# Optimization experiments

Measured on AMD Instinct MI355X. Metric: run time of the kernel, lower is better.

The kernel has to match this reference:

```python
import jax, jax.numpy as jnp
import numpy as np

N_NODES = 200000
D = 128            # in_channels
B_GRAPHS = 512     # batch_size
STEPS = 3          # processing_steps


def setup_inputs() -> dict:
    key = jax.random.key(0)
    k = jax.random.split(key, 6)
    x = jax.random.normal(k[0], (N_NODES, D), dtype=jnp.float32)
    batch = jnp.sort(jax.random.randint(k[1], (N_NODES,), 0, B_GRAPHS, dtype=jnp.int64))
    s = 0.1
    W_ih = jax.random.normal(k[2], (3 * D, 2 * D), dtype=jnp.float32) * s
    W_hh = jax.random.normal(k[3], (3 * D, D), dtype=jnp.float32) * s
    b_ih = jax.random.normal(k[4], (3 * D,), dtype=jnp.float32) * s
    b_hh = jax.random.normal(k[5], (3 * D,), dtype=jnp.float32) * s
    return {"x": x, "batch": batch, "batch_size": B_GRAPHS,
            "W_ih": W_ih, "W_hh": W_hh, "b_ih": b_ih, "b_hh": b_hh}


def _gru_cell(inp, h, W_ih, W_hh, b_ih, b_hh):
    # inp: [B, 2d], h: [B, d]; PyTorch GRU gate order: r, z, n
    gi = inp @ W_ih.T + b_ih  # [B, 3d]
    gh = h @ W_hh.T + b_hh    # [B, 3d]
    gi_r, gi_z, gi_n = jnp.split(gi, 3, axis=-1)
    gh_r, gh_z, gh_n = jnp.split(gh, 3, axis=-1)
    r = jax.nn.sigmoid(gi_r + gh_r)
    z = jax.nn.sigmoid(gi_z + gh_z)
    n = jnp.tanh(gi_n + r * gh_n)
    return (1.0 - z) * n + z * h


def reference(x, batch, batch_size, W_ih, W_hh, b_ih, b_hh):
    B = batch_size
    d = x.shape[1]
    h = jnp.zeros((B, d), dtype=x.dtype)
    q_star = jnp.zeros((B, 2 * d), dtype=x.dtype)
    for _ in range(STEPS):
        h = _gru_cell(q_star, h, W_ih, W_hh, b_ih, b_hh)
        q = h  # num_layers=1: output == new hidden state
        e = jnp.sum(x * q[batch], axis=-1)  # [N]
        m = jax.ops.segment_max(e, batch, num_segments=B)
        ex = jnp.exp(e - m[batch])
        s = jax.ops.segment_sum(ex, batch, num_segments=B)
        a = ex / (s[batch] + 1e-16)  # segment softmax weights [N]
        r = jax.ops.segment_sum(a[:, None] * x, batch, num_segments=B)  # [B, d]
        q_star = jnp.concatenate([q, r], axis=-1)
    return q_star
```

## Files before the change

kernel.cpp:

```cpp
#include <hip/hip_runtime.h>
#include <math.h>

constexpr int D = 128;
constexpr int B = 512;
constexpr int STEPS = 3;
constexpr int NW_IH = 3 * D * 2 * D;
constexpr int NW_HH = 3 * D * D;

__device__ __forceinline__ float sigmoidf_(float x) { return 1.f / (1.f + __expf(-x)); }
__device__ __forceinline__ float bflo(unsigned int u) { return __uint_as_float(u << 16); }
__device__ __forceinline__ float bfhi(unsigned int u) { return __uint_as_float(u & 0xffff0000u); }
__device__ __forceinline__ unsigned short f2bf_rn(float f) {
    unsigned int u = __float_as_uint(f);
    u += 0x7fffu + ((u >> 16) & 1u);
    return (unsigned short)(u >> 16);
}

__global__ __launch_bounds__(256) void k_prep(const float* __restrict__ Wih,
        const float* __restrict__ Whh, const int* __restrict__ batch, int n,
        unsigned short* __restrict__ wih_bf, unsigned short* __restrict__ whh_bf,
        int* __restrict__ seg) {
    int i = blockIdx.x * blockDim.x + threadIdx.x;
    if (i < NW_IH) wih_bf[i] = f2bf_rn(Wih[i]);
    else if (i < NW_IH + NW_HH) whh_bf[i - NW_IH] = f2bf_rn(Whh[i - NW_IH]);
    if (i <= B) {
        int lo = 0, hi = n;
        while (lo < hi) { int mid = (lo + hi) >> 1; if (batch[mid] < i) lo = mid + 1; else hi = mid; }
        seg[i] = lo;
    }
}

__global__ __launch_bounds__(1024, 8) void k_set2set(
        const float* __restrict__ x,
        const unsigned short* __restrict__ wih_bf,
        const unsigned short* __restrict__ whh_bf,
        const float* __restrict__ bih, const float* __restrict__ bhh,
        const int* __restrict__ seg, float* __restrict__ out) {
    __shared__ float s_q[2 * D];
    __shared__ float s_h[D];
    __shared__ float s_gi[3 * D], s_gh[3 * D];
    __shared__ float sm[32], sl[32];
    __shared__ float s_M, s_inv;
    __shared__ float rpart[16][D];

    const int b = blockIdx.x;
    const int tid = threadIdx.x;
    const int start = seg[b], end = seg[b + 1];
    const int lane32 = tid & 31;
    const int hw = tid >> 5;

    if (tid < 2 * D) s_q[tid] = 0.f;
    if (tid < D) s_h[tid] = 0.f;
    __syncthreads();

    for (int step = 0; step < STEPS; ++step) {
        if (tid < 3 * D) {
            const int t = tid;
            float gi = bih[t], gh = bhh[t];
            const uint4* wr = (const uint4*)(wih_bf + (size_t)t * (2 * D));
#pragma unroll 2
            for (int c = 0; c < (2 * D) / 8; ++c) {
                uint4 w = wr[c];
                const float* q = &s_q[c * 8];
                gi = fmaf(bflo(w.x), q[0], gi); gi = fmaf(bfhi(w.x), q[1], gi);
                gi = fmaf(bflo(w.y), q[2], gi); gi = fmaf(bfhi(w.y), q[3], gi);
                gi = fmaf(bflo(w.z), q[4], gi); gi = fmaf(bfhi(w.z), q[5], gi);
                gi = fmaf(bflo(w.w), q[6], gi); gi = fmaf(bfhi(w.w), q[7], gi);
            }
            const uint4* vr = (const uint4*)(whh_bf + (size_t)t * D);
#pragma unroll 2
            for (int c = 0; c < D / 8; ++c) {
                uint4 w = vr[c];
                const float* hh = &s_h[c * 8];
                gh = fmaf(bflo(w.x), hh[0], gh); gh = fmaf(bfhi(w.x), hh[1], gh);
                gh = fmaf(bflo(w.y), hh[2], gh); gh = fmaf(bfhi(w.y), hh[3], gh);
                gh = fmaf(bflo(w.z), hh[4], gh); gh = fmaf(bfhi(w.z), hh[5], gh);
                gh = fmaf(bflo(w.w), hh[6], gh); gh = fmaf(bfhi(w.w), hh[7], gh);
            }
            s_gi[t] = gi; s_gh[t] = gh;
        }
        __syncthreads();
        if (tid < D) {
            const int t = tid;
            float r  = sigmoidf_(s_gi[t] + s_gh[t]);
            float z  = sigmoidf_(s_gi[D + t] + s_gh[D + t]);
            float nn = tanhf(s_gi[2 * D + t] + r * s_gh[2 * D + t]);
            float hn = (1.f - z) * nn + z * s_h[t];
            s_h[t] = hn;
            s_q[t] = hn;
        }
        __syncthreads();

        const float4 qf = *(const float4*)&s_h[lane32 * 4];
        float m_run = -INFINITY, l_run = 0.f;
        float4 acc = {0.f, 0.f, 0.f, 0.f};
        for (int node = start + hw; node < end; node += 32) {
            float4 xv = ((const float4*)(x + (size_t)node * D))[lane32];
            float p = fmaf(xv.x, qf.x, fmaf(xv.y, qf.y, fmaf(xv.z, qf.z, xv.w * qf.w)));
            p += __shfl_xor(p, 16, 64);
            p += __shfl_xor(p, 8, 64);
            p += __shfl_xor(p, 4, 64);
            p += __shfl_xor(p, 2, 64);
            p += __shfl_xor(p, 1, 64);
            float nm = fmaxf(m_run, p);
            float scale = __expf(m_run - nm);
            float a = __expf(p - nm);
            l_run = fmaf(l_run, scale, a);
            acc.x = fmaf(acc.x, scale, a * xv.x);
            acc.y = fmaf(acc.y, scale, a * xv.y);
            acc.z = fmaf(acc.z, scale, a * xv.z);
            acc.w = fmaf(acc.w, scale, a * xv.w);
            m_run = nm;
        }
        if (lane32 == 0) { sm[hw] = m_run; sl[hw] = l_run; }
        __syncthreads();
        if (tid == 0) {
            float M = -INFINITY;
            for (int i = 0; i < 32; ++i) M = fmaxf(M, sm[i]);
            float L = 0.f;
            for (int i = 0; i < 32; ++i)
                L += (sm[i] == -INFINITY) ? 0.f : sl[i] * __expf(sm[i] - M);
            s_M = M;
            s_inv = 1.f / (L + 1e-16f);
        }
        __syncthreads();
        const float fac = (m_run == -INFINITY) ? 0.f : __expf(m_run - s_M);
        acc.x *= fac; acc.y *= fac; acc.z *= fac; acc.w *= fac;
        acc.x += __shfl_down(acc.x, 32, 64);
        acc.y += __shfl_down(acc.y, 32, 64);
        acc.z += __shfl_down(acc.z, 32, 64);
        acc.w += __shfl_down(acc.w, 32, 64);
        const int wave = tid >> 6;
        const int lane64 = tid & 63;
        if (lane64 < 32) ((float4*)rpart[wave])[lane64] = acc;
        __syncthreads();
        if (tid < D) {
            float v = 0.f;
#pragma unroll
            for (int w = 0; w < 16; ++w) v += rpart[w][tid];
            s_q[D + tid] = v * s_inv;
        }
        __syncthreads();
    }

    if (tid < 2 * D) out[(size_t)b * (2 * D) + tid] = s_q[tid];
}

extern "C" void kernel_launch(void* const* d_in, const int* in_sizes, int n_in,
                              void* d_out, int out_size, void* d_ws, size_t ws_size,
                              hipStream_t stream) {
    const float* x    = (const float*)d_in[0];
    const int*   batch= (const int*)d_in[1];
    const float* Wih  = (const float*)d_in[3];
    const float* Whh  = (const float*)d_in[4];
    const float* bih  = (const float*)d_in[5];
    const float* bhh  = (const float*)d_in[6];
    const int n = in_sizes[0] / D;

    char* ws = (char*)d_ws;
    int* seg = (int*)ws;
    unsigned short* wih_bf = (unsigned short*)(ws + 4096);
    unsigned short* whh_bf = (unsigned short*)(ws + 4096 + (size_t)NW_IH * 2);

    const int total = NW_IH + NW_HH;
    k_prep<<<(total + 255) / 256, 256, 0, stream>>>(Wih, Whh, batch, n, wih_bf, whh_bf, seg);
    k_set2set<<<B, 1024, 0, stream>>>(x, wih_bf, whh_bf, bih, bhh, seg, (float*)d_out);
}
```

Before: 250.8 us.

## Split fused Set2Set kernel into per-step GRU and split-segment attention kernels

Replaces the single persistent kernel (one 1024-thread block per graph running all steps) with a loop of launches per step: a GRU kernel, an attention kernel that splits each graph's nodes into four chunks across 2048 blocks of 256 threads and writes partial softmax stats, and a final combine kernel. The aim is higher occupancy and better load balance for the memory-bound node scan over x. The GRU dot products now use four independent accumulators to shorten the FMA dependency chain. The cost is seven extra launches and partial results round-tripping through global memory between steps.

```diff
diff --git a/kernel.cpp b/kernel.cpp
--- a/kernel.cpp
+++ b/kernel.cpp
@@ -30,120 +30,175 @@
     }
 }
 
-__global__ __launch_bounds__(1024, 8) void k_set2set(
-        const float* __restrict__ x,
+__global__ __launch_bounds__(384) void k_cg(
         const unsigned short* __restrict__ wih_bf,
         const unsigned short* __restrict__ whh_bf,
         const float* __restrict__ bih, const float* __restrict__ bhh,
-        const int* __restrict__ seg, float* __restrict__ out) {
+        float* __restrict__ g_h,
+        const float* __restrict__ Pm, const float* __restrict__ Pl,
+        const float* __restrict__ Pacc, int first) {
     __shared__ float s_q[2 * D];
     __shared__ float s_h[D];
     __shared__ float s_gi[3 * D], s_gh[3 * D];
-    __shared__ float sm[32], sl[32];
-    __shared__ float s_M, s_inv;
-    __shared__ float rpart[16][D];
-
-    const int b = blockIdx.x;
+    const int g = blockIdx.x;
+    const int t = threadIdx.x;
+
+    if (t < D) {
+        float hp = first ? 0.f : g_h[(size_t)g * D + t];
+        s_h[t] = hp;
+        s_q[t] = hp;
+        float r = 0.f;
+        if (!first) {
+            float m0 = Pm[g * 4 + 0], m1 = Pm[g * 4 + 1];
+            float m2 = Pm[g * 4 + 2], m3 = Pm[g * 4 + 3];
+            float M = fmaxf(fmaxf(m0, m1), fmaxf(m2, m3));
+            float w0 = (m0 == -INFINITY) ? 0.f : __expf(m0 - M);
+            float w1 = (m1 == -INFINITY) ? 0.f : __expf(m1 - M);
+            float w2 = (m2 == -INFINITY) ? 0.f : __expf(m2 - M);
+            float w3 = (m3 == -INFINITY) ? 0.f : __expf(m3 - M);
+            float l = w0 * Pl[g * 4 + 0] + w1 * Pl[g * 4 + 1]
+                    + w2 * Pl[g * 4 + 2] + w3 * Pl[g * 4 + 3];
+            float inv = 1.f / (l + 1e-16f);
+            r = (w0 * Pacc[(size_t)(g * 4 + 0) * D + t]
+               + w1 * Pacc[(size_t)(g * 4 + 1) * D + t]
+               + w2 * Pacc[(size_t)(g * 4 + 2) * D + t]
+               + w3 * Pacc[(size_t)(g * 4 + 3) * D + t]) * inv;
+        }
+        s_q[D + t] = r;
+    }
+    __syncthreads();
+
+    {
+        float a0 = bih[t], a1 = 0.f, a2 = 0.f, a3 = 0.f;
+        const uint4* wr = (const uint4*)(wih_bf + (size_t)t * (2 * D));
+#pragma unroll 4
+        for (int c = 0; c < (2 * D) / 8; ++c) {
+            uint4 w = wr[c];
+            const float* q = &s_q[c * 8];
+            a0 = fmaf(bflo(w.x), q[0], a0); a0 = fmaf(bfhi(w.x), q[1], a0);
+            a1 = fmaf(bflo(w.y), q[2], a1); a1 = fmaf(bfhi(w.y), q[3], a1);
+            a2 = fmaf(bflo(w.z), q[4], a2); a2 = fmaf(bfhi(w.z), q[5], a2);
+            a3 = fmaf(bflo(w.w), q[6], a3); a3 = fmaf(bfhi(w.w), q[7], a3);
+        }
+        s_gi[t] = (a0 + a1) + (a2 + a3);
+        float b0 = bhh[t], b1 = 0.f, b2 = 0.f, b3 = 0.f;
+        const uint4* vr = (const uint4*)(whh_bf + (size_t)t * D);
+#pragma unroll 4
+        for (int c = 0; c < D / 8; ++c) {
+            uint4 w = vr[c];
+            const float* hh = &s_h[c * 8];
+            b0 = fmaf(bflo(w.x), hh[0], b0); b0 = fmaf(bfhi(w.x), hh[1], b0);
+            b1 = fmaf(bflo(w.y), hh[2], b1); b1 = fmaf(bfhi(w.y), hh[3], b1);
+            b2 = fmaf(bflo(w.z), hh[4], b2); b2 = fmaf(bfhi(w.z), hh[5], b2);
+            b3 = fmaf(bflo(w.w), hh[6], b3); b3 = fmaf(bfhi(w.w), hh[7], b3);
+        }
+        s_gh[t] = (b0 + b1) + (b2 + b3);
+    }
+    __syncthreads();
+
+    if (t < D) {
+        float r  = sigmoidf_(s_gi[t] + s_gh[t]);
+        float z  = sigmoidf_(s_gi[D + t] + s_gh[D + t]);
+        float nn = tanhf(s_gi[2 * D + t] + r * s_gh[2 * D + t]);
+        float hn = (1.f - z) * nn + z * s_h[t];
+        g_h[(size_t)g * D + t] = hn;
+    }
+}
+
+__global__ __launch_bounds__(256, 8) void k_attn_p(const float* __restrict__ x,
+        const float* __restrict__ g_h, const int* __restrict__ seg,
+        float* __restrict__ Pm, float* __restrict__ Pl,
+        float* __restrict__ Pacc) {
+    const int bid = blockIdx.x;
+    const int g = bid >> 2, j = bid & 3;
+    const int s = seg[g], e = seg[g + 1];
+    const int len = e - s;
+    const int qs = s + (len * j) / 4;
+    const int qe = s + (len * (j + 1)) / 4;
+
     const int tid = threadIdx.x;
-    const int start = seg[b], end = seg[b + 1];
     const int lane32 = tid & 31;
     const int hw = tid >> 5;
 
-    if (tid < 2 * D) s_q[tid] = 0.f;
-    if (tid < D) s_h[tid] = 0.f;
-    __syncthreads();
-
-    for (int step = 0; step < STEPS; ++step) {
-        if (tid < 3 * D) {
-            const int t = tid;
-            float gi = bih[t], gh = bhh[t];
-            const uint4* wr = (const uint4*)(wih_bf + (size_t)t * (2 * D));
-#pragma unroll 2
-            for (int c = 0; c < (2 * D) / 8; ++c) {
-                uint4 w = wr[c];
-                const float* q = &s_q[c * 8];
-                gi = fmaf(bflo(w.x), q[0], gi); gi = fmaf(bfhi(w.x), q[1], gi);
-                gi = fmaf(bflo(w.y), q[2], gi); gi = fmaf(bfhi(w.y), q[3], gi);
-                gi = fmaf(bflo(w.z), q[4], gi); gi = fmaf(bfhi(w.z), q[5], gi);
-                gi = fmaf(bflo(w.w), q[6], gi); gi = fmaf(bfhi(w.w), q[7], gi);
-            }
-            const uint4* vr = (const uint4*)(whh_bf + (size_t)t * D);
-#pragma unroll 2
-            for (int c = 0; c < D / 8; ++c) {
-                uint4 w = vr[c];
-                const float* hh = &s_h[c * 8];
-                gh = fmaf(bflo(w.x), hh[0], gh); gh = fmaf(bfhi(w.x), hh[1], gh);
-                gh = fmaf(bflo(w.y), hh[2], gh); gh = fmaf(bfhi(w.y), hh[3], gh);
-                gh = fmaf(bflo(w.z), hh[4], gh); gh = fmaf(bfhi(w.z), hh[5], gh);
-                gh = fmaf(bflo(w.w), hh[6], gh); gh = fmaf(bfhi(w.w), hh[7], gh);
-            }
-            s_gi[t] = gi; s_gh[t] = gh;
-        }
-        __syncthreads();
-        if (tid < D) {
-            const int t = tid;
-            float r  = sigmoidf_(s_gi[t] + s_gh[t]);
-            float z  = sigmoidf_(s_gi[D + t] + s_gh[D + t]);
-            float nn = tanhf(s_gi[2 * D + t] + r * s_gh[2 * D + t]);
-            float hn = (1.f - z) * nn + z * s_h[t];
-            s_h[t] = hn;
-            s_q[t] = hn;
-        }
-        __syncthreads();
-
-        const float4 qf = *(const float4*)&s_h[lane32 * 4];
-        float m_run = -INFINITY, l_run = 0.f;
-        float4 acc = {0.f, 0.f, 0.f, 0.f};
-        for (int node = start + hw; node < end; node += 32) {
-            float4 xv = ((const float4*)(x + (size_t)node * D))[lane32];
-            float p = fmaf(xv.x, qf.x, fmaf(xv.y, qf.y, fmaf(xv.z, qf.z, xv.w * qf.w)));
-            p += __shfl_xor(p, 16, 64);
-            p += __shfl_xor(p, 8, 64);
-            p += __shfl_xor(p, 4, 64);
-            p += __shfl_xor(p, 2, 64);
-            p += __shfl_xor(p, 1, 64);
-            float nm = fmaxf(m_run, p);
-            float scale = __expf(m_run - nm);
-            float a = __expf(p - nm);
-            l_run = fmaf(l_run, scale, a);
-            acc.x = fmaf(acc.x, scale, a * xv.x);
-            acc.y = fmaf(acc.y, scale, a * xv.y);
-            acc.z = fmaf(acc.z, scale, a * xv.z);
-            acc.w = fmaf(acc.w, scale, a * xv.w);
-            m_run = nm;
-        }
-        if (lane32 == 0) { sm[hw] = m_run; sl[hw] = l_run; }
-        __syncthreads();
-        if (tid == 0) {
-            float M = -INFINITY;
-            for (int i = 0; i < 32; ++i) M = fmaxf(M, sm[i]);
-            float L = 0.f;
-            for (int i = 0; i < 32; ++i)
-                L += (sm[i] == -INFINITY) ? 0.f : sl[i] * __expf(sm[i] - M);
-            s_M = M;
-            s_inv = 1.f / (L + 1e-16f);
-        }
-        __syncthreads();
-        const float fac = (m_run == -INFINITY) ? 0.f : __expf(m_run - s_M);
-        acc.x *= fac; acc.y *= fac; acc.z *= fac; acc.w *= fac;
-        acc.x += __shfl_down(acc.x, 32, 64);
-        acc.y += __shfl_down(acc.y, 32, 64);
-        acc.z += __shfl_down(acc.z, 32, 64);
-        acc.w += __shfl_down(acc.w, 32, 64);
-        const int wave = tid >> 6;
-        const int lane64 = tid & 63;
-        if (lane64 < 32) ((float4*)rpart[wave])[lane64] = acc;
-        __syncthreads();
-        if (tid < D) {
-            float v = 0.f;
+    const float4 qf = ((const float4*)(g_h + (size_t)g * D))[lane32];
+
+    float m_run = -INFINITY, l_run = 0.f;
+    float4 acc = {0.f, 0.f, 0.f, 0.f};
+    for (int node = qs + hw; node < qe; node += 8) {
+        float4 xv = ((const float4*)(x + (size_t)node * D))[lane32];
+        float p = fmaf(xv.x, qf.x, fmaf(xv.y, qf.y, fmaf(xv.z, qf.z, xv.w * qf.w)));
+        p += __shfl_xor(p, 16, 64);
+        p += __shfl_xor(p, 8, 64);
+        p += __shfl_xor(p, 4, 64);
+        p += __shfl_xor(p, 2, 64);
+        p += __shfl_xor(p, 1, 64);
+        float nm = fmaxf(m_run, p);
+        float scale = __expf(m_run - nm);
+        float a = __expf(p - nm);
+        l_run = fmaf(l_run, scale, a);
+        acc.x = fmaf(acc.x, scale, a * xv.x);
+        acc.y = fmaf(acc.y, scale, a * xv.y);
+        acc.z = fmaf(acc.z, scale, a * xv.z);
+        acc.w = fmaf(acc.w, scale, a * xv.w);
+        m_run = nm;
+    }
+
+    __shared__ float sm[8], sl[8];
+    __shared__ float s_M;
+    if (lane32 == 0) { sm[hw] = m_run; sl[hw] = l_run; }
+    __syncthreads();
+    if (tid == 0) {
+        float M = -INFINITY;
 #pragma unroll
-            for (int w = 0; w < 16; ++w) v += rpart[w][tid];
-            s_q[D + tid] = v * s_inv;
-        }
-        __syncthreads();
-    }
-
-    if (tid < 2 * D) out[(size_t)b * (2 * D) + tid] = s_q[tid];
+        for (int i = 0; i < 8; ++i) M = fmaxf(M, sm[i]);
+        float L = 0.f;
+#pragma unroll
+        for (int i = 0; i < 8; ++i)
+            L += (sm[i] == -INFINITY) ? 0.f : sl[i] * __expf(sm[i] - M);
+        s_M = M;
+        Pm[bid] = M;
+        Pl[bid] = L;
+    }
+    __syncthreads();
+    const float fac = (m_run == -INFINITY) ? 0.f : __expf(m_run - s_M);
+    acc.x *= fac; acc.y *= fac; acc.z *= fac; acc.w *= fac;
+    acc.x += __shfl_down(acc.x, 32, 64);
+    acc.y += __shfl_down(acc.y, 32, 64);
+    acc.z += __shfl_down(acc.z, 32, 64);
+    acc.w += __shfl_down(acc.w, 32, 64);
+
+    __shared__ float rpart[4][D];
+    const int wave = tid >> 6;
+    const int lane64 = tid & 63;
+    if (lane64 < 32) ((float4*)rpart[wave])[lane64] = acc;
+    __syncthreads();
+    if (tid < D) {
+        float v = (rpart[0][tid] + rpart[1][tid]) + (rpart[2][tid] + rpart[3][tid]);
+        Pacc[(size_t)bid * D + tid] = v;
+    }
+}
+
+__global__ __launch_bounds__(128) void k_out(const float* __restrict__ g_h,
+        const float* __restrict__ Pm, const float* __restrict__ Pl,
+        const float* __restrict__ Pacc, float* __restrict__ out) {
+    const int g = blockIdx.x;
+    const int t = threadIdx.x;
+    out[(size_t)g * (2 * D) + t] = g_h[(size_t)g * D + t];
+    float m0 = Pm[g * 4 + 0], m1 = Pm[g * 4 + 1];
+    float m2 = Pm[g * 4 + 2], m3 = Pm[g * 4 + 3];
+    float M = fmaxf(fmaxf(m0, m1), fmaxf(m2, m3));
+    float w0 = (m0 == -INFINITY) ? 0.f : __expf(m0 - M);
+    float w1 = (m1 == -INFINITY) ? 0.f : __expf(m1 - M);
+    float w2 = (m2 == -INFINITY) ? 0.f : __expf(m2 - M);
+    float w3 = (m3 == -INFINITY) ? 0.f : __expf(m3 - M);
+    float l = w0 * Pl[g * 4 + 0] + w1 * Pl[g * 4 + 1]
+            + w2 * Pl[g * 4 + 2] + w3 * Pl[g * 4 + 3];
+    float inv = 1.f / (l + 1e-16f);
+    float r = (w0 * Pacc[(size_t)(g * 4 + 0) * D + t]
+             + w1 * Pacc[(size_t)(g * 4 + 1) * D + t]
+             + w2 * Pacc[(size_t)(g * 4 + 2) * D + t]
+             + w3 * Pacc[(size_t)(g * 4 + 3) * D + t]) * inv;
+    out[(size_t)g * (2 * D) + D + t] = r;
 }
 
 extern "C" void kernel_launch(void* const* d_in, const int* in_sizes, int n_in,
@@ -158,11 +213,21 @@
     const int n = in_sizes[0] / D;
 
     char* ws = (char*)d_ws;
-    int* seg = (int*)ws;
-    unsigned short* wih_bf = (unsigned short*)(ws + 4096);
-    unsigned short* whh_bf = (unsigned short*)(ws + 4096 + (size_t)NW_IH * 2);
+    int* seg              = (int*)(ws);
+    unsigned short* wih_bf= (unsigned short*)(ws + 4096);
+    unsigned short* whh_bf= (unsigned short*)(ws + 200704);
+    float* g_h            = (float*)(ws + 299008);
+    float* Pm             = (float*)(ws + 561152);
+    float* Pl             = (float*)(ws + 569344);
+    float* Pacc           = (float*)(ws + 577536);
 
     const int total = NW_IH + NW_HH;
     k_prep<<<(total + 255) / 256, 256, 0, stream>>>(Wih, Whh, batch, n, wih_bf, whh_bf, seg);
-    k_set2set<<<B, 1024, 0, stream>>>(x, wih_bf, whh_bf, bih, bhh, seg, (float*)d_out);
-}
+
+    for (int s = 0; s < STEPS; ++s) {
+        k_cg<<<B, 384, 0, stream>>>(wih_bf, whh_bf, bih, bhh, g_h, Pm, Pl, Pacc,
+                                    s == 0 ? 1 : 0);
+        k_attn_p<<<4 * B, 256, 0, stream>>>(x, g_h, seg, Pm, Pl, Pacc);
+    }
+    k_out<<<B, 128, 0, stream>>>(g_h, Pm, Pl, Pacc, (float*)d_out);
+}
```

After: 268.5 us. 7.1% more time.

## Halve block size, split GRU dot-product accumulators, parallelize softmax merge

Applied to the files above, without the earlier changes.

The set2set kernel now runs with 512 threads per block instead of 1024, so each half-wave handles every 16th node and the per-wave partial buffers shrink to match. The GRU matvec uses four independent accumulators with deeper unrolling to break the FMA dependency chain. The final cross-half-wave online-softmax merge becomes a shuffle-based log-step reduction instead of a serial loop in one thread. With fewer threads per block, each block streams its graph's nodes with less parallelism per block, though the lighter blocks may allow more blocks per CU.

```diff
diff --git a/kernel.cpp b/kernel.cpp
--- a/kernel.cpp
+++ b/kernel.cpp
@@ -30,7 +30,7 @@
     }
 }
 
-__global__ __launch_bounds__(1024, 8) void k_set2set(
+__global__ __launch_bounds__(512, 8) void k_set2set(
         const float* __restrict__ x,
         const unsigned short* __restrict__ wih_bf,
         const unsigned short* __restrict__ whh_bf,
@@ -39,9 +39,9 @@
     __shared__ float s_q[2 * D];
     __shared__ float s_h[D];
     __shared__ float s_gi[3 * D], s_gh[3 * D];
-    __shared__ float sm[32], sl[32];
+    __shared__ float sm[16], sl[16];
     __shared__ float s_M, s_inv;
-    __shared__ float rpart[16][D];
+    __shared__ float rpart[8][D];
 
     const int b = blockIdx.x;
     const int tid = threadIdx.x;
@@ -56,28 +56,30 @@
     for (int step = 0; step < STEPS; ++step) {
         if (tid < 3 * D) {
             const int t = tid;
-            float gi = bih[t], gh = bhh[t];
+            float a0 = bih[t], a1 = 0.f, a2 = 0.f, a3 = 0.f;
             const uint4* wr = (const uint4*)(wih_bf + (size_t)t * (2 * D));
-#pragma unroll 2
+#pragma unroll 4
             for (int c = 0; c < (2 * D) / 8; ++c) {
                 uint4 w = wr[c];
                 const float* q = &s_q[c * 8];
-                gi = fmaf(bflo(w.x), q[0], gi); gi = fmaf(bfhi(w.x), q[1], gi);
-                gi = fmaf(bflo(w.y), q[2], gi); gi = fmaf(bfhi(w.y), q[3], gi);
-                gi = fmaf(bflo(w.z), q[4], gi); gi = fmaf(bfhi(w.z), q[5], gi);
-                gi = fmaf(bflo(w.w), q[6], gi); gi = fmaf(bfhi(w.w), q[7], gi);
+                a0 = fmaf(bflo(w.x), q[0], a0); a0 = fmaf(bfhi(w.x), q[1], a0);
+                a1 = fmaf(bflo(w.y), q[2], a1); a1 = fmaf(bfhi(w.y), q[3], a1);
+                a2 = fmaf(bflo(w.z), q[4], a2); a2 = fmaf(bfhi(w.z), q[5], a2);
+                a3 = fmaf(bflo(w.w), q[6], a3); a3 = fmaf(bfhi(w.w), q[7], a3);
             }
+            s_gi[t] = (a0 + a1) + (a2 + a3);
+            float b0 = bhh[t], b1 = 0.f, b2 = 0.f, b3 = 0.f;
             const uint4* vr = (const uint4*)(whh_bf + (size_t)t * D);
-#pragma unroll 2
+#pragma unroll 4
             for (int c = 0; c < D / 8; ++c) {
                 uint4 w = vr[c];
                 const float* hh = &s_h[c * 8];
-                gh = fmaf(bflo(w.x), hh[0], gh); gh = fmaf(bfhi(w.x), hh[1], gh);
-                gh = fmaf(bflo(w.y), hh[2], gh); gh = fmaf(bfhi(w.y), hh[3], gh);
-                gh = fmaf(bflo(w.z), hh[4], gh); gh = fmaf(bfhi(w.z), hh[5], gh);
-                gh = fmaf(bflo(w.w), hh[6], gh); gh = fmaf(bfhi(w.w), hh[7], gh);
+                b0 = fmaf(bflo(w.x), hh[0], b0); b0 = fmaf(bfhi(w.x), hh[1], b0);
+                b1 = fmaf(bflo(w.y), hh[2], b1); b1 = fmaf(bfhi(w.y), hh[3], b1);
+                b2 = fmaf(bflo(w.z), hh[4], b2); b2 = fmaf(bfhi(w.z), hh[5], b2);
+                b3 = fmaf(bflo(w.w), hh[6], b3); b3 = fmaf(bfhi(w.w), hh[7], b3);
             }
-            s_gi[t] = gi; s_gh[t] = gh;
+            s_gh[t] = (b0 + b1) + (b2 + b3);
         }
         __syncthreads();
         if (tid < D) {
@@ -94,7 +96,7 @@
         const float4 qf = *(const float4*)&s_h[lane32 * 4];
         float m_run = -INFINITY, l_run = 0.f;
         float4 acc = {0.f, 0.f, 0.f, 0.f};
-        for (int node = start + hw; node < end; node += 32) {
+        for (int node = start + hw; node < end; node += 16) {
             float4 xv = ((const float4*)(x + (size_t)node * D))[lane32];
             float p = fmaf(xv.x, qf.x, fmaf(xv.y, qf.y, fmaf(xv.z, qf.z, xv.w * qf.w)));
             p += __shfl_xor(p, 16, 64);
@@ -114,14 +116,18 @@
         }
         if (lane32 == 0) { sm[hw] = m_run; sl[hw] = l_run; }
         __syncthreads();
-        if (tid == 0) {
-            float M = -INFINITY;
-            for (int i = 0; i < 32; ++i) M = fmaxf(M, sm[i]);
-            float L = 0.f;
-            for (int i = 0; i < 32; ++i)
-                L += (sm[i] == -INFINITY) ? 0.f : sl[i] * __expf(sm[i] - M);
-            s_M = M;
-            s_inv = 1.f / (L + 1e-16f);
+        if (tid < 64) {
+            float m = sm[tid & 15], l = sl[tid & 15];
+#pragma unroll
+            for (int s = 8; s >= 1; s >>= 1) {
+                float mo = __shfl_xor(m, s, 64);
+                float lo = __shfl_xor(l, s, 64);
+                float nm2 = fmaxf(m, mo);
+                float t1 = (m  == -INFINITY) ? 0.f : l  * __expf(m  - nm2);
+                float t2 = (mo == -INFINITY) ? 0.f : lo * __expf(mo - nm2);
+                l = t1 + t2; m = nm2;
+            }
+            if (tid == 0) { s_M = m; s_inv = 1.f / (l + 1e-16f); }
         }
         __syncthreads();
         const float fac = (m_run == -INFINITY) ? 0.f : __expf(m_run - s_M);
@@ -137,7 +143,7 @@
         if (tid < D) {
             float v = 0.f;
 #pragma unroll
-            for (int w = 0; w < 16; ++w) v += rpart[w][tid];
+            for (int w = 0; w < 8; ++w) v += rpart[w][tid];
             s_q[D + tid] = v * s_inv;
         }
         __syncthreads();
@@ -164,5 +170,5 @@
 
     const int total = NW_IH + NW_HH;
     k_prep<<<(total + 255) / 256, 256, 0, stream>>>(Wih, Whh, batch, n, wih_bf, whh_bf, seg);
-    k_set2set<<<B, 1024, 0, stream>>>(x, wih_bf, whh_bf, bih, bhh, seg, (float*)d_out);
+    k_set2set<<<B, 512, 0, stream>>>(x, wih_bf, whh_bf, bih, bhh, seg, (float*)d_out);
 }
```

Result: no change. 253.3 us (+1.0%).
